# Kernel optimization log

Measured on AMD Instinct MI355X. Metric: run time of the kernel, lower is better.

## Reference

```python
import jax, jax.numpy as jnp
import numpy as np

M = 16                      # multiplicity of each irrep block
INV3 = 1.0 / np.sqrt(3.0)   # w3j(1,1,0) component-normalized
INV2 = 1.0 / np.sqrt(2.0)   # w3j(1,1,1) component-normalized
A0 = 1.0 / np.sqrt(2.0 * M) # fan-in norm for 0e outputs (2 paths x mul 16)
A1 = 1.0 / np.sqrt(3.0 * M) # fan-in norm for 1o outputs (3 paths x mul 16)


def setup_inputs() -> dict:
    E, N, ED, HID = 100000, 10000, 32, 128
    WNUM = 2 * M * (2 * M) + 3 * M * M  # 1792 per-edge TP weights
    ks = jax.random.split(jax.random.key(0), 10)
    return {
        "dst": jax.random.randint(ks[0], (E,), 0, N),
        "x_src": jax.random.normal(ks[1], (E, 4 * M), jnp.float32),   # 16x0e+16x1o
        "x_dst": jax.random.normal(ks[2], (N, 4 * M), jnp.float32),
        "sh": jax.random.normal(ks[3], (E, 4), jnp.float32),          # 1x0e+1x1o
        "edge_attr": jax.random.normal(ks[4], (E, ED), jnp.float32),
        "We1": jax.random.normal(ks[5], (ED, HID), jnp.float32) / np.sqrt(ED),
        "be1": jnp.zeros((HID,), jnp.float32),
        "We2": jax.random.normal(ks[6], (HID, WNUM), jnp.float32) / np.sqrt(HID),
        "be2": jnp.zeros((WNUM,), jnp.float32),
        "Wr0": jax.random.normal(ks[7], (M, 2 * M), jnp.float32),     # 16x0e -> 32x0e
        "Wr1": jax.random.normal(ks[8], (M, M), jnp.float32),         # 16x1o -> 16x1o
    }


def _forward(dst, x_src, x_dst, sh, edge_attr, We1, be1, We2, be2, Wr0, Wr1):
    E = x_src.shape[0]
    N = x_dst.shape[0]
    o0 = 2 * M  # 32x0e tp output (scalars + gates)

    # edge MLP -> per-edge tensor-product weights [E, 1792]
    w = jax.nn.relu(edge_attr @ We1 + be1) @ We2 + be2
    i = 0
    w_ss = w[:, i:i + M * o0].reshape(E, M, o0); i += M * o0   # 0e x 0e -> 0e
    w_vv0 = w[:, i:i + M * o0].reshape(E, M, o0); i += M * o0  # 1o x 1o -> 0e
    w_sv = w[:, i:i + M * M].reshape(E, M, M); i += M * M      # 0e x 1o -> 1o
    w_vs = w[:, i:i + M * M].reshape(E, M, M); i += M * M      # 1o x 0e -> 1o
    w_vv1 = w[:, i:i + M * M].reshape(E, M, M)                 # 1o x 1o -> 1o

    s1 = x_src[:, :M]                       # [E, 16]
    v1 = x_src[:, M:].reshape(E, M, 3)      # [E, 16, 3]
    s2 = sh[:, 0]                           # [E]
    v2 = sh[:, 1:4]                         # [E, 3]

    # fully-connected tensor product with per-edge weights
    out0 = A0 * (jnp.einsum('em,emo->eo', s1 * s2[:, None], w_ss)
                 + INV3 * jnp.einsum('emc,ec,emo->eo', v1, v2, w_vv0))  # [E, 32]
    cross = jnp.cross(v1, v2[:, None, :])   # [E, 16, 3]
    out1 = A1 * (jnp.einsum('em,ec,emo->eoc', s1, v2, w_sv)
                 + jnp.einsum('emc,e,emo->eoc', v1, s2, w_vs)
                 + INV2 * jnp.einsum('emc,emo->eoc', cross, w_vv1))     # [E, 16, 3]
    msg = jnp.concatenate([out0, out1.reshape(E, -1)], axis=1)          # [E, 80]

    # scatter-mean over destination nodes
    ssum = jax.ops.segment_sum(msg, dst, num_segments=N)
    cnt = jax.ops.segment_sum(jnp.ones((E,), msg.dtype), dst, num_segments=N)
    msg = ssum / jnp.maximum(cnt, 1.0)[:, None]                          # [N, 80]

    # residual equivariant linear on x_dst
    sd = x_dst[:, :M]
    vd = x_dst[:, M:].reshape(N, M, 3)
    res0 = (sd @ Wr0) / np.sqrt(M)                                       # [N, 32]
    res1 = jnp.einsum('nmc,mo->noc', vd, Wr1) / np.sqrt(M)               # [N, 16, 3]
    msg = msg + jnp.concatenate([res0, res1.reshape(N, -1)], axis=1)

    # gate nonlinearity: relu(scalars), sigmoid(gates) * gated vectors
    scalars = jax.nn.relu(msg[:, :M])
    gates = jax.nn.sigmoid(msg[:, M:2 * M])
    gated = msg[:, 2 * M:].reshape(N, M, 3) * gates[:, :, None]
    return jnp.concatenate([scalars, gated.reshape(N, -1)], axis=1)      # [N, 64]


def reference(dst, x_src, x_dst, sh, edge_attr, We1, be1, We2, be2, Wr0, Wr1):
    return _forward(dst, x_src, x_dst, sh, edge_attr, We1, be1, We2, be2, Wr0, Wr1)
```

## Files before the change

kernel.cpp:

```cpp
#include <hip/hip_runtime.h>
#include <math.h>

#define WNUM 1792
#define HID 128

#define INV3C 0.5773502691896258f
#define INV2C 0.7071067811865476f
#define A0C   0.17677669529663687f
#define A1C   0.14433756729740643f
#define MAXDEG 64

typedef short bf8 __attribute__((ext_vector_type(8)));
typedef _Float16 f16x8 __attribute__((ext_vector_type(8)));
typedef _Float16 f16x4 __attribute__((ext_vector_type(4)));
typedef float f32x4 __attribute__((ext_vector_type(4)));

__device__ inline unsigned short f2bf(float f) {
  union { float f; unsigned u; } v; v.f = f;
  unsigned r = v.u + 0x7FFFu + ((v.u >> 16) & 1u);
  return (unsigned short)(r >> 16);
}
__device__ inline float bf2f(unsigned short h) {
  union { unsigned u; float f; } v; v.u = ((unsigned)h) << 16;
  return v.f;
}
__device__ inline float wscale(int t) {
  if (t < 32) return A0C;
  if (t < 64) return A0C * INV3C;
  if (t < 96) return A1C;
  return A1C * INV2C;
}

__global__ __launch_bounds__(256) void prep_kernel(
    const float* __restrict__ We1, const float* __restrict__ We2,
    const float* __restrict__ be2,
    unsigned short* __restrict__ we1x, _Float16* __restrict__ we2h,
    float* __restrict__ be2p, int* __restrict__ cntp, int N)
{
  int i = blockIdx.x * 256 + threadIdx.x;
  if (i < 28672) {
    int t = i >> 8, c = (i >> 6) & 3, lane = i & 63;
    int quad = lane >> 4, l15 = lane & 15;
    int col = t * 16 + l15;
    float sc = wscale(t);
    f16x8 v;
    #pragma unroll
    for (int j = 0; j < 8; ++j) {
      int k = c * 32 + quad * 8 + j;
      v[j] = (_Float16)(We2[(size_t)k * WNUM + col] * sc);
    }
    *(f16x8*)(we2h + (size_t)t * 2048 + c * 512 + lane * 8) = v;
  } else if (i < 29184) {
    int q = i - 28672;
    int c1 = q >> 6, lane = q & 63;
    int quad = lane >> 4, l15 = lane & 15;
    int col = c1 * 16 + l15;
    bf8 hh, ll;
    #pragma unroll
    for (int j = 0; j < 8; ++j) {
      int k = quad * 8 + j;
      float v = We1[k * HID + col];
      unsigned short hi = f2bf(v);
      hh[j] = (short)hi;
      ll[j] = (short)f2bf(v - bf2f(hi));
    }
    *(bf8*)(we1x + c1 * 1024 + lane * 8) = hh;
    *(bf8*)(we1x + c1 * 1024 + 512 + lane * 8) = ll;
  } else if (i < 30976) {
    int q = i - 29184;
    int t = q >> 4, l16 = q & 15;
    be2p[(t >> 1) * 32 + l16 * 2 + (t & 1)] = be2[q] * wscale(t);
  } else if (i < 30976 + N) {
    cntp[i - 30976] = 0;
  }
}

__device__ inline void chains2(const f16x8* a0, const f16x8* a1,
    f16x8 b0, f16x8 b1, f16x8 b2, f16x8 b3,
    f16x8 b4, f16x8 b5, f16x8 b6, f16x8 b7,
    float2 bias, f32x4* wa, f32x4* wb)
{
  f32x4 ca0 = {bias.x, bias.x, bias.x, bias.x};
  f32x4 cb0 = {bias.y, bias.y, bias.y, bias.y};
  f32x4 ca1 = ca0, cb1 = cb0;
  ca0 = __builtin_amdgcn_mfma_f32_16x16x32_f16(a0[0], b0, ca0, 0, 0, 0);
  cb0 = __builtin_amdgcn_mfma_f32_16x16x32_f16(a0[0], b4, cb0, 0, 0, 0);
  ca1 = __builtin_amdgcn_mfma_f32_16x16x32_f16(a1[0], b0, ca1, 0, 0, 0);
  cb1 = __builtin_amdgcn_mfma_f32_16x16x32_f16(a1[0], b4, cb1, 0, 0, 0);
  ca0 = __builtin_amdgcn_mfma_f32_16x16x32_f16(a0[1], b1, ca0, 0, 0, 0);
  cb0 = __builtin_amdgcn_mfma_f32_16x16x32_f16(a0[1], b5, cb0, 0, 0, 0);
  ca1 = __builtin_amdgcn_mfma_f32_16x16x32_f16(a1[1], b1, ca1, 0, 0, 0);
  cb1 = __builtin_amdgcn_mfma_f32_16x16x32_f16(a1[1], b5, cb1, 0, 0, 0);
  ca0 = __builtin_amdgcn_mfma_f32_16x16x32_f16(a0[2], b2, ca0, 0, 0, 0);
  cb0 = __builtin_amdgcn_mfma_f32_16x16x32_f16(a0[2], b6, cb0, 0, 0, 0);
  ca1 = __builtin_amdgcn_mfma_f32_16x16x32_f16(a1[2], b2, ca1, 0, 0, 0);
  cb1 = __builtin_amdgcn_mfma_f32_16x16x32_f16(a1[2], b6, cb1, 0, 0, 0);
  ca0 = __builtin_amdgcn_mfma_f32_16x16x32_f16(a0[3], b3, ca0, 0, 0, 0);
  cb0 = __builtin_amdgcn_mfma_f32_16x16x32_f16(a0[3], b7, cb0, 0, 0, 0);
  ca1 = __builtin_amdgcn_mfma_f32_16x16x32_f16(a1[3], b3, ca1, 0, 0, 0);
  cb1 = __builtin_amdgcn_mfma_f32_16x16x32_f16(a1[3], b7, cb1, 0, 0, 0);
  wa[0] = ca0; wb[0] = cb0; wa[1] = ca1; wb[1] = cb1;
}

__device__ inline void pair_mm(const _Float16* bL, const float* bp, int p,
                               const f16x8 (&af)[2][4], f32x4* wa, f32x4* wb)
{
  f16x8 b0 = *(const f16x8*)(bL);
  f16x8 b1 = *(const f16x8*)(bL + 512);
  f16x8 b2 = *(const f16x8*)(bL + 1024);
  f16x8 b3 = *(const f16x8*)(bL + 1536);
  f16x8 b4 = *(const f16x8*)(bL + 2048);
  f16x8 b5 = *(const f16x8*)(bL + 2560);
  f16x8 b6 = *(const f16x8*)(bL + 3072);
  f16x8 b7 = *(const f16x8*)(bL + 3584);
  float2 bias2 = *(const float2*)(bp + p * 32);
  chains2(af[0], af[1], b0, b1, b2, b3, b4, b5, b6, b7, bias2, wa, wb);
}

template <bool MSG>
__global__ __launch_bounds__(512, 2) void edge_kernel(
    const float* __restrict__ ea, const float* __restrict__ xsrc,
    const float* __restrict__ sh, const int* __restrict__ dst,
    const float* __restrict__ be1,
    const unsigned short* __restrict__ we1x, const _Float16* __restrict__ we2h,
    const float* __restrict__ be2p,
    float* __restrict__ outp, int* __restrict__ eidx, int* __restrict__ cntp, int E)
{
  const int lane = threadIdx.x & 63;
  const int w    = threadIdx.x >> 6;
  const int quad = lane >> 4;
  const int l16  = lane & 15;
  const int eb   = (blockIdx.x * 8 + w) * 32;

  __shared__ union SMem {
    _Float16 h[8][16][136];
    _Float16 B[4][4096];
  } uS;
  __shared__ _Float16 s1h_s[8][16][32];
  __shared__ _Float16 v1h_s[8][16][3][32];
  __shared__ float4 vq_s[8][32];

  #define STAGE_PAIR(p) { \
    const _Float16* gsrc_ = we2h + (size_t)(p) * 4096; \
    _Float16* ldst_ = &uS.B[(p) & 3][0]; \
    __builtin_amdgcn_global_load_lds( \
      (const __attribute__((address_space(1))) void*)(gsrc_ + w * 512 + lane * 8), \
      (__attribute__((address_space(3))) void*)(ldst_ + w * 512), 16, 0, 0); \
  }

  if (lane < 32) {
    int ge = eb + lane;
    if (ge < E) {
      int node = dst[ge];
      int pos = atomicAdd(cntp + node, 1);
      if (MSG) { if (pos < MAXDEG) eidx[node * MAXDEG + pos] = ge; }
    }
  }

  {
    int e2 = lane >> 1, mg = lane & 1;
    int ge = eb + e2;
    if (ge < E) {
      const float* xp = xsrc + (size_t)ge * 64;
      float4 sq0 = *(const float4*)(xp + mg * 8);
      float4 sq1 = *(const float4*)(xp + mg * 8 + 4);
      float s1a[8] = {sq0.x,sq0.y,sq0.z,sq0.w,sq1.x,sq1.y,sq1.z,sq1.w};
      const float* vp = xp + 16 + mg * 24;
      float la[24];
      #pragma unroll
      for (int qv = 0; qv < 6; ++qv) {
        float4 t = *(const float4*)(vp + qv * 4);
        la[qv*4+0] = t.x; la[qv*4+1] = t.y; la[qv*4+2] = t.z; la[qv*4+3] = t.w;
      }
      float4 shq = *(const float4*)(sh + (size_t)ge * 4);
      float s2 = shq.x, v2x = shq.y, v2y = shq.z, v2z = shq.w;
      #pragma unroll
      for (int mi = 0; mi < 8; ++mi) {
        int m = mg * 8 + mi;
        float v1x = la[mi*3], v1y = la[mi*3+1], v1z = la[mi*3+2];
        s1h_s[w][m][e2] = (_Float16)s1a[mi];
        v1h_s[w][m][0][e2] = (_Float16)v1x;
        v1h_s[w][m][1][e2] = (_Float16)v1y;
        v1h_s[w][m][2][e2] = (_Float16)v1z;
      }
      if (mg == 0) vq_s[w][e2] = make_float4(v2x, v2y, v2z, s2);
    } else {
      #pragma unroll
      for (int mi = 0; mi < 8; ++mi) {
        int m = mg * 8 + mi;
        s1h_s[w][m][e2] = (_Float16)0.f;
        v1h_s[w][m][0][e2] = (_Float16)0.f;
        v1h_s[w][m][1][e2] = (_Float16)0.f;
        v1h_s[w][m][2][e2] = (_Float16)0.f;
      }
      if (mg == 0) vq_s[w][e2] = make_float4(0,0,0,0);
    }
  }

  f16x8 af[2][4];
  {
    const unsigned short* wb1 = we1x + lane * 8;
    #pragma unroll
    for (int g = 0; g < 2; ++g) {
      bf8 ah, al;
      {
        int gea = eb + g * 16 + l16; if (gea > E - 1) gea = E - 1;
        const float* ep = ea + (size_t)gea * 32 + quad * 8;
        float4 p0 = *(const float4*)ep;
        float4 p1 = *(const float4*)(ep + 4);
        float pv[8] = {p0.x,p0.y,p0.z,p0.w,p1.x,p1.y,p1.z,p1.w};
        #pragma unroll
        for (int j = 0; j < 8; ++j) {
          unsigned short hi = f2bf(pv[j]);
          ah[j] = (short)hi;
          al[j] = (short)f2bf(pv[j] - bf2f(hi));
        }
      }
      #pragma unroll 2
      for (int c = 0; c < 8; ++c) {
        bf8 bh = *(const bf8*)(wb1 + c * 1024);
        bf8 bl = *(const bf8*)(wb1 + c * 1024 + 512);
        float bias = be1[c * 16 + l16];
        f32x4 hc = {bias, bias, bias, bias};
        hc = __builtin_amdgcn_mfma_f32_16x16x32_bf16(al, bh, hc, 0, 0, 0);
        hc = __builtin_amdgcn_mfma_f32_16x16x32_bf16(ah, bl, hc, 0, 0, 0);
        hc = __builtin_amdgcn_mfma_f32_16x16x32_bf16(ah, bh, hc, 0, 0, 0);
        #pragma unroll
        for (int r = 0; r < 4; ++r)
          uS.h[w][quad * 4 + r][c * 16 + l16] = (_Float16)fmaxf(hc[r], 0.f);
      }
      #pragma unroll
      for (int ch = 0; ch < 4; ++ch)
        af[g][ch] = *(const f16x8*)&uS.h[w][l16][ch * 32 + quad * 8];
      asm volatile("s_waitcnt lgkmcnt(0)" ::: "memory");
      __builtin_amdgcn_sched_barrier(0);
    }
  }
  __syncthreads();

  STAGE_PAIR(0)
  STAGE_PAIR(1)
  __syncthreads();

  const float* bp = be2p + l16 * 2;
  float m0a[2][4] = {{0,0,0,0},{0,0,0,0}}, m0b[2][4] = {{0,0,0,0},{0,0,0,0}};

  {
    float s2v[2][4];
    #pragma unroll
    for (int g = 0; g < 2; ++g)
      #pragma unroll
      for (int r = 0; r < 4; ++r)
        s2v[g][r] = vq_s[w][g * 16 + quad * 4 + r].w;

    #pragma unroll 1
    for (int i = 0; i < 16; i += 2) {
      STAGE_PAIR(i + 2)
      STAGE_PAIR(i + 3)
      f32x4 wa[2], wb[2];
      pair_mm(&uS.B[i & 3][lane * 8], bp, i, af, wa, wb);
      #pragma unroll
      for (int g = 0; g < 2; ++g) {
        f16x4 fv = *(const f16x4*)&s1h_s[w][i][g * 16 + quad * 4];
        #pragma unroll
        for (int r = 0; r < 4; ++r) {
          float f = (float)fv[r] * s2v[g][r];
          m0a[g][r] = fmaf(wa[g][r], f, m0a[g][r]);
          m0b[g][r] = fmaf(wb[g][r], f, m0b[g][r]);
        }
      }
      pair_mm(&uS.B[(i + 1) & 3][lane * 8], bp, i + 1, af, wa, wb);
      #pragma unroll
      for (int g = 0; g < 2; ++g) {
        f16x4 fv = *(const f16x4*)&s1h_s[w][i + 1][g * 16 + quad * 4];
        #pragma unroll
        for (int r = 0; r < 4; ++r) {
          float f = (float)fv[r] * s2v[g][r];
          m0a[g][r] = fmaf(wa[g][r], f, m0a[g][r]);
          m0b[g][r] = fmaf(wb[g][r], f, m0b[g][r]);
        }
      }
      __syncthreads();
    }
  }

  {
    float v2xv[2][4], v2yv[2][4], v2zv[2][4];
    #pragma unroll
    for (int g = 0; g < 2; ++g)
      #pragma unroll
      for (int r = 0; r < 4; ++r) {
        float4 q = vq_s[w][g * 16 + quad * 4 + r];
        v2xv[g][r] = q.x; v2yv[g][r] = q.y; v2zv[g][r] = q.z;
      }

    #pragma unroll 1
    for (int i = 0; i < 16; i += 2) {
      int pg = 16 + i;
      STAGE_PAIR(pg + 2)
      STAGE_PAIR(pg + 3)
      f32x4 wa[2], wb[2];
      pair_mm(&uS.B[pg & 3][lane * 8], bp, pg, af, wa, wb);
      #pragma unroll
      for (int g = 0; g < 2; ++g) {
        f16x4 xA = *(const f16x4*)&v1h_s[w][i][0][g * 16 + quad * 4];
        f16x4 yA = *(const f16x4*)&v1h_s[w][i][1][g * 16 + quad * 4];
        f16x4 zA = *(const f16x4*)&v1h_s[w][i][2][g * 16 + quad * 4];
        #pragma unroll
        for (int r = 0; r < 4; ++r) {
          float f = fmaf((float)zA[r], v2zv[g][r],
                    fmaf((float)yA[r], v2yv[g][r], (float)xA[r] * v2xv[g][r]));
          m0a[g][r] = fmaf(wa[g][r], f, m0a[g][r]);
          m0b[g][r] = fmaf(wb[g][r], f, m0b[g][r]);
        }
      }
      pair_mm(&uS.B[(pg + 1) & 3][lane * 8], bp, pg + 1, af, wa, wb);
      #pragma unroll
      for (int g = 0; g < 2; ++g) {
        f16x4 xA = *(const f16x4*)&v1h_s[w][i + 1][0][g * 16 + quad * 4];
        f16x4 yA = *(const f16x4*)&v1h_s[w][i + 1][1][g * 16 + quad * 4];
        f16x4 zA = *(const f16x4*)&v1h_s[w][i + 1][2][g * 16 + quad * 4];
        #pragma unroll
        for (int r = 0; r < 4; ++r) {
          float f = fmaf((float)zA[r], v2zv[g][r],
                    fmaf((float)yA[r], v2yv[g][r], (float)xA[r] * v2xv[g][r]));
          m0a[g][r] = fmaf(wa[g][r], f, m0a[g][r]);
          m0b[g][r] = fmaf(wb[g][r], f, m0b[g][r]);
        }
      }
      __syncthreads();
    }
  }

  #pragma unroll
  for (int g = 0; g < 2; ++g)
    #pragma unroll
    for (int r = 0; r < 4; ++r) {
      int ge = eb + g * 16 + quad * 4 + r;
      if (ge < E) {
        if (MSG) {
          float* mp = outp + (size_t)ge * 80;
          mp[l16]      = m0a[g][r];
          mp[16 + l16] = m0b[g][r];
        } else {
          float* ap = outp + (size_t)dst[ge] * 80;
          atomicAdd(ap + l16,      m0a[g][r]);
          atomicAdd(ap + 16 + l16, m0b[g][r]);
        }
      }
    }

  float sg[2][4] = {{0,0,0,0},{0,0,0,0}};
  #pragma unroll 1
  for (int i = 0; i < 8; i += 2) {
    int pg = 32 + i;
    STAGE_PAIR(pg + 2)
    STAGE_PAIR(pg + 3)
    f32x4 wa[2], wb[2];
    pair_mm(&uS.B[pg & 3][lane * 8], bp, pg, af, wa, wb);
    #pragma unroll
    for (int g = 0; g < 2; ++g) {
      f16x4 sA = *(const f16x4*)&s1h_s[w][2*i][g * 16 + quad * 4];
      f16x4 sB = *(const f16x4*)&s1h_s[w][2*i + 1][g * 16 + quad * 4];
      #pragma unroll
      for (int r = 0; r < 4; ++r)
        sg[g][r] = fmaf(wb[g][r], (float)sB[r], fmaf(wa[g][r], (float)sA[r], sg[g][r]));
    }
    pair_mm(&uS.B[(pg + 1) & 3][lane * 8], bp, pg + 1, af, wa, wb);
    #pragma unroll
    for (int g = 0; g < 2; ++g) {
      f16x4 sA = *(const f16x4*)&s1h_s[w][2*i + 2][g * 16 + quad * 4];
      f16x4 sB = *(const f16x4*)&s1h_s[w][2*i + 3][g * 16 + quad * 4];
      #pragma unroll
      for (int r = 0; r < 4; ++r)
        sg[g][r] = fmaf(wb[g][r], (float)sB[r], fmaf(wa[g][r], (float)sA[r], sg[g][r]));
    }
    __syncthreads();
  }
  float4 vq[2][4];
  #pragma unroll
  for (int g = 0; g < 2; ++g)
    #pragma unroll
    for (int r = 0; r < 4; ++r) vq[g][r] = vq_s[w][g * 16 + quad * 4 + r];

  float m1x[2][4], m1y[2][4], m1z[2][4];
  #pragma unroll
  for (int g = 0; g < 2; ++g)
    #pragma unroll
    for (int r = 0; r < 4; ++r) {
      m1x[g][r] = sg[g][r] * vq[g][r].x;
      m1y[g][r] = sg[g][r] * vq[g][r].y;
      m1z[g][r] = sg[g][r] * vq[g][r].z;
    }

  #pragma unroll
  for (int sec = 0; sec < 2; ++sec) {
    float ux[2][4] = {{0,0,0,0},{0,0,0,0}}, uy[2][4] = {{0,0,0,0},{0,0,0,0}},
          uz[2][4] = {{0,0,0,0},{0,0,0,0}};
    int base = 40 + sec * 8;
    #pragma unroll 1
    for (int i = 0; i < 8; i += 2) {
      int pg = base + i;
      if (pg + 2 < 56) STAGE_PAIR(pg + 2)
      if (pg + 3 < 56) STAGE_PAIR(pg + 3)
      f32x4 wa[2], wb[2];
      pair_mm(&uS.B[pg & 3][lane * 8], bp, pg, af, wa, wb);
      #pragma unroll
      for (int g = 0; g < 2; ++g) {
        f16x4 xA = *(const f16x4*)&v1h_s[w][2*i][0][g*16 + quad*4];
        f16x4 xB = *(const f16x4*)&v1h_s[w][2*i+1][0][g*16 + quad*4];
        f16x4 yA = *(const f16x4*)&v1h_s[w][2*i][1][g*16 + quad*4];
        f16x4 yB = *(const f16x4*)&v1h_s[w][2*i+1][1][g*16 + quad*4];
        f16x4 zA = *(const f16x4*)&v1h_s[w][2*i][2][g*16 + quad*4];
        f16x4 zB = *(const f16x4*)&v1h_s[w][2*i+1][2][g*16 + quad*4];
        #pragma unroll
        for (int r = 0; r < 4; ++r) {
          ux[g][r] = fmaf(wb[g][r], (float)xB[r], fmaf(wa[g][r], (float)xA[r], ux[g][r]));
          uy[g][r] = fmaf(wb[g][r], (float)yB[r], fmaf(wa[g][r], (float)yA[r], uy[g][r]));
          uz[g][r] = fmaf(wb[g][r], (float)zB[r], fmaf(wa[g][r], (float)zA[r], uz[g][r]));
        }
      }
      pair_mm(&uS.B[(pg + 1) & 3][lane * 8], bp, pg + 1, af, wa, wb);
      #pragma unroll
      for (int g = 0; g < 2; ++g) {
        f16x4 xA = *(const f16x4*)&v1h_s[w][2*i+2][0][g*16 + quad*4];
        f16x4 xB = *(const f16x4*)&v1h_s[w][2*i+3][0][g*16 + quad*4];
        f16x4 yA = *(const f16x4*)&v1h_s[w][2*i+2][1][g*16 + quad*4];
        f16x4 yB = *(const f16x4*)&v1h_s[w][2*i+3][1][g*16 + quad*4];
        f16x4 zA = *(const f16x4*)&v1h_s[w][2*i+2][2][g*16 + quad*4];
        f16x4 zB = *(const f16x4*)&v1h_s[w][2*i+3][2][g*16 + quad*4];
        #pragma unroll
        for (int r = 0; r < 4; ++r) {
          ux[g][r] = fmaf(wb[g][r], (float)xB[r], fmaf(wa[g][r], (float)xA[r], ux[g][r]));
          uy[g][r] = fmaf(wb[g][r], (float)yB[r], fmaf(wa[g][r], (float)yA[r], uy[g][r]));
          uz[g][r] = fmaf(wb[g][r], (float)zB[r], fmaf(wa[g][r], (float)zA[r], uz[g][r]));
        }
      }
      __syncthreads();
    }
    if (sec == 0) {
      #pragma unroll
      for (int g = 0; g < 2; ++g)
        #pragma unroll
        for (int r = 0; r < 4; ++r) {
          m1x[g][r] = fmaf(vq[g][r].w, ux[g][r], m1x[g][r]);
          m1y[g][r] = fmaf(vq[g][r].w, uy[g][r], m1y[g][r]);
          m1z[g][r] = fmaf(vq[g][r].w, uz[g][r], m1z[g][r]);
        }
    } else {
      #pragma unroll
      for (int g = 0; g < 2; ++g)
        #pragma unroll
        for (int r = 0; r < 4; ++r) {
          m1x[g][r] = fmaf(uy[g][r], vq[g][r].z, m1x[g][r]);
          m1x[g][r] = fmaf(-uz[g][r], vq[g][r].y, m1x[g][r]);
          m1y[g][r] = fmaf(uz[g][r], vq[g][r].x, m1y[g][r]);
          m1y[g][r] = fmaf(-ux[g][r], vq[g][r].z, m1y[g][r]);
          m1z[g][r] = fmaf(ux[g][r], vq[g][r].y, m1z[g][r]);
          m1z[g][r] = fmaf(-uy[g][r], vq[g][r].x, m1z[g][r]);
        }
    }
  }

  #pragma unroll
  for (int g = 0; g < 2; ++g)
    #pragma unroll
    for (int r = 0; r < 4; ++r) {
      int ge = eb + g * 16 + quad * 4 + r;
      if (ge < E) {
        if (MSG) {
          float* mp = outp + (size_t)ge * 80;
          mp[32 + l16*3 + 0] = m1x[g][r];
          mp[32 + l16*3 + 1] = m1y[g][r];
          mp[32 + l16*3 + 2] = m1z[g][r];
        } else {
          float* ap = outp + (size_t)dst[ge] * 80;
          atomicAdd(ap + 32 + l16*3 + 0, m1x[g][r]);
          atomicAdd(ap + 32 + l16*3 + 1, m1y[g][r]);
          atomicAdd(ap + 32 + l16*3 + 2, m1z[g][r]);
        }
      }
    }
  #undef STAGE_PAIR
}

__global__ __launch_bounds__(128) void node_gather_kernel(
    const float* __restrict__ msg, const int* __restrict__ eidx,
    const int* __restrict__ cntp,
    const float* __restrict__ xdst, const float* __restrict__ Wr0,
    const float* __restrict__ Wr1, float* __restrict__ out, int N)
{
  int n = blockIdx.x;
  if (n >= N) return;
  int j = threadIdx.x;
  int c0 = cntp[n];
  int deg = c0 < MAXDEG ? c0 : MAXDEG;
  float inv = 1.0f / fmaxf((float)c0, 1.0f);
  __shared__ float s_sum[80];
  if (j < 80) {
    float s = 0.f;
    const int* ep = eidx + (size_t)n * MAXDEG;
    int i = 0;
    for (; i + 1 < deg; i += 2) {
      int e0 = ep[i], e1 = ep[i + 1];
      s += msg[(size_t)e0 * 80 + j] + msg[(size_t)e1 * 80 + j];
    }
    if (i < deg) s += msg[(size_t)ep[i] * 80 + j];
    s_sum[j] = s * inv;
  }
  __syncthreads();
  if (j >= 64) return;
  const float* xd = xdst + (size_t)n * 64;
  float* op = out + (size_t)n * 64;
  if (j < 16) {
    float s = 0.f;
    #pragma unroll
    for (int m = 0; m < 16; ++m) s = fmaf(xd[m], Wr0[m * 32 + j], s);
    op[j] = fmaxf(s_sum[j] + 0.25f * s, 0.f);
  } else {
    int jj = j - 16;
    int o = (jj * 86) >> 8;
    int c = jj - o * 3;
    float tg = 0.f, v = 0.f;
    #pragma unroll
    for (int m = 0; m < 16; ++m) {
      tg = fmaf(xd[m], Wr0[m * 32 + 16 + o], tg);
      v  = fmaf(xd[16 + m * 3 + c], Wr1[m * 16 + o], v);
    }
    float g = 1.0f / (1.0f + expf(-(s_sum[16 + o] + 0.25f * tg)));
    op[16 + jj] = (s_sum[32 + jj] + 0.25f * v) * g;
  }
}

__global__ __launch_bounds__(256) void node_kernel(
    const float* __restrict__ accn, const int* __restrict__ cntp,
    const float* __restrict__ xdst, const float* __restrict__ Wr0,
    const float* __restrict__ Wr1, float* __restrict__ out, int N)
{
  int idx = blockIdx.x * 256 + threadIdx.x;
  int n = idx >> 6, j = idx & 63;
  if (n >= N) return;
  float inv = 1.0f / fmaxf((float)cntp[n], 1.0f);
  const float* ap = accn + (size_t)n * 80;
  const float* xd = xdst + (size_t)n * 64;
  float* op = out + (size_t)n * 64;
  if (j < 16) {
    float s = 0.f;
    #pragma unroll
    for (int m = 0; m < 16; ++m) s = fmaf(xd[m], Wr0[m * 32 + j], s);
    op[j] = fmaxf(ap[j] * inv + 0.25f * s, 0.f);
  } else {
    int jj = j - 16;
    int o = (jj * 86) >> 8;
    int c = jj - o * 3;
    float tg = 0.f, v = 0.f;
    #pragma unroll
    for (int m = 0; m < 16; ++m) {
      tg = fmaf(xd[m], Wr0[m * 32 + 16 + o], tg);
      v  = fmaf(xd[16 + m * 3 + c], Wr1[m * 16 + o], v);
    }
    float g = 1.0f / (1.0f + expf(-(ap[16 + o] * inv + 0.25f * tg)));
    op[16 + jj] = (ap[32 + jj] * inv + 0.25f * v) * g;
  }
}

extern "C" void kernel_launch(void* const* d_in, const int* in_sizes, int n_in,
                              void* d_out, int out_size, void* d_ws, size_t ws_size,
                              hipStream_t stream)
{
  const int*   dst  = (const int*)d_in[0];
  const float* xsrc = (const float*)d_in[1];
  const float* xdst = (const float*)d_in[2];
  const float* sh   = (const float*)d_in[3];
  const float* ea   = (const float*)d_in[4];
  const float* We1  = (const float*)d_in[5];
  const float* be1  = (const float*)d_in[6];
  const float* We2  = (const float*)d_in[7];
  const float* be2  = (const float*)d_in[8];
  const float* Wr0  = (const float*)d_in[9];
  const float* Wr1  = (const float*)d_in[10];
  const int E = in_sizes[0];
  const int N = in_sizes[2] / 64;

  char* ws = (char*)d_ws;
  _Float16* we2h = (_Float16*)ws;
  unsigned short* we1x = (unsigned short*)(ws + 458752);
  float* be2p = (float*)(ws + 475136);
  int*   cntp = (int*)(ws + 482560);
  size_t off = 482560 + (size_t)N * 4;
  off = (off + 15) & ~(size_t)15;

  size_t need_msg = off + (size_t)N * MAXDEG * 4 + (size_t)E * 80 * 4;
  bool use_msg = (ws_size >= need_msg);

  prep_kernel<<<(30976 + N + 255) / 256, 256, 0, stream>>>(We1, We2, be2,
      we1x, we2h, be2p, cntp, N);

  if (use_msg) {
    int* eidx = (int*)(ws + off);
    float* msg = (float*)(ws + off + (size_t)N * MAXDEG * 4);
    edge_kernel<true><<<(E + 255) / 256, 512, 0, stream>>>(ea, xsrc, sh, dst, be1,
        we1x, we2h, be2p, msg, eidx, cntp, E);
    node_gather_kernel<<<N, 128, 0, stream>>>(msg, eidx, cntp, xdst, Wr0, Wr1,
        (float*)d_out, N);
  } else {
    float* accn = (float*)(ws + off);
    hipMemsetAsync(accn, 0, (size_t)N * 320, stream);
    edge_kernel<false><<<(E + 255) / 256, 512, 0, stream>>>(ea, xsrc, sh, dst, be1,
        we1x, we2h, be2p, accn, (int*)nullptr, cntp, E);
    node_kernel<<<((size_t)N * 64 + 255) / 256, 256, 0, stream>>>(accn, cntp,
        xdst, Wr0, Wr1, (float*)d_out, N);
  }
}
```

Baseline: 206.4 us.

## Read We2 tiles directly from global memory instead of LDS staging, halve block size

Drops the cooperative global_load_lds staging of the per-edge TP weight matrix (We2) into a four-slot LDS ring buffer. Each wave now loads its B fragments straight from global memory, relying on L1/L2 caching of the small shared weight table. This removes the per-iteration __syncthreads barriers and frees the staging LDS. Blocks shrink from 8 to 4 waves to raise occupancy and scheduling flexibility. The cost is more global and cache traffic per wave and exposed load latency before each MFMA chain, since there is no longer any software prefetch.

```diff
diff --git a/kernel.cpp b/kernel.cpp
--- a/kernel.cpp
+++ b/kernel.cpp
@@ -102,23 +102,23 @@
   wa[0] = ca0; wb[0] = cb0; wa[1] = ca1; wb[1] = cb1;
 }
 
-__device__ inline void pair_mm(const _Float16* bL, const float* bp, int p,
+__device__ inline void pair_mm(const _Float16* __restrict__ bG, const float* bp, int p,
                                const f16x8 (&af)[2][4], f32x4* wa, f32x4* wb)
 {
-  f16x8 b0 = *(const f16x8*)(bL);
-  f16x8 b1 = *(const f16x8*)(bL + 512);
-  f16x8 b2 = *(const f16x8*)(bL + 1024);
-  f16x8 b3 = *(const f16x8*)(bL + 1536);
-  f16x8 b4 = *(const f16x8*)(bL + 2048);
-  f16x8 b5 = *(const f16x8*)(bL + 2560);
-  f16x8 b6 = *(const f16x8*)(bL + 3072);
-  f16x8 b7 = *(const f16x8*)(bL + 3584);
+  f16x8 b0 = *(const f16x8*)(bG);
+  f16x8 b1 = *(const f16x8*)(bG + 512);
+  f16x8 b2 = *(const f16x8*)(bG + 1024);
+  f16x8 b3 = *(const f16x8*)(bG + 1536);
+  f16x8 b4 = *(const f16x8*)(bG + 2048);
+  f16x8 b5 = *(const f16x8*)(bG + 2560);
+  f16x8 b6 = *(const f16x8*)(bG + 3072);
+  f16x8 b7 = *(const f16x8*)(bG + 3584);
   float2 bias2 = *(const float2*)(bp + p * 32);
   chains2(af[0], af[1], b0, b1, b2, b3, b4, b5, b6, b7, bias2, wa, wb);
 }
 
 template <bool MSG>
-__global__ __launch_bounds__(512, 2) void edge_kernel(
+__global__ __launch_bounds__(256, 2) void edge_kernel(
     const float* __restrict__ ea, const float* __restrict__ xsrc,
     const float* __restrict__ sh, const int* __restrict__ dst,
     const float* __restrict__ be1,
@@ -130,23 +130,12 @@
   const int w    = threadIdx.x >> 6;
   const int quad = lane >> 4;
   const int l16  = lane & 15;
-  const int eb   = (blockIdx.x * 8 + w) * 32;
-
-  __shared__ union SMem {
-    _Float16 h[8][16][136];
-    _Float16 B[4][4096];
-  } uS;
-  __shared__ _Float16 s1h_s[8][16][32];
-  __shared__ _Float16 v1h_s[8][16][3][32];
-  __shared__ float4 vq_s[8][32];
-
-  #define STAGE_PAIR(p) { \
-    const _Float16* gsrc_ = we2h + (size_t)(p) * 4096; \
-    _Float16* ldst_ = &uS.B[(p) & 3][0]; \
-    __builtin_amdgcn_global_load_lds( \
-      (const __attribute__((address_space(1))) void*)(gsrc_ + w * 512 + lane * 8), \
-      (__attribute__((address_space(3))) void*)(ldst_ + w * 512), 16, 0, 0); \
-  }
+  const int eb   = (blockIdx.x * 4 + w) * 32;
+
+  __shared__ _Float16 h_s[4][16][136];
+  __shared__ _Float16 s1h_s[4][16][32];
+  __shared__ _Float16 v1h_s[4][16][3][32];
+  __shared__ float4 vq_s[4][32];
 
   if (lane < 32) {
     int ge = eb + lane;
@@ -227,22 +216,18 @@
         hc = __builtin_amdgcn_mfma_f32_16x16x32_bf16(ah, bh, hc, 0, 0, 0);
         #pragma unroll
         for (int r = 0; r < 4; ++r)
-          uS.h[w][quad * 4 + r][c * 16 + l16] = (_Float16)fmaxf(hc[r], 0.f);
+          h_s[w][quad * 4 + r][c * 16 + l16] = (_Float16)fmaxf(hc[r], 0.f);
       }
       #pragma unroll
       for (int ch = 0; ch < 4; ++ch)
-        af[g][ch] = *(const f16x8*)&uS.h[w][l16][ch * 32 + quad * 8];
+        af[g][ch] = *(const f16x8*)&h_s[w][l16][ch * 32 + quad * 8];
       asm volatile("s_waitcnt lgkmcnt(0)" ::: "memory");
       __builtin_amdgcn_sched_barrier(0);
     }
   }
-  __syncthreads();
-
-  STAGE_PAIR(0)
-  STAGE_PAIR(1)
-  __syncthreads();
 
   const float* bp = be2p + l16 * 2;
+  const _Float16* bG0 = we2h + lane * 8;
   float m0a[2][4] = {{0,0,0,0},{0,0,0,0}}, m0b[2][4] = {{0,0,0,0},{0,0,0,0}};
 
   {
@@ -255,10 +240,8 @@
 
     #pragma unroll 1
     for (int i = 0; i < 16; i += 2) {
-      STAGE_PAIR(i + 2)
-      STAGE_PAIR(i + 3)
       f32x4 wa[2], wb[2];
-      pair_mm(&uS.B[i & 3][lane * 8], bp, i, af, wa, wb);
+      pair_mm(bG0 + (size_t)i * 4096, bp, i, af, wa, wb);
       #pragma unroll
       for (int g = 0; g < 2; ++g) {
         f16x4 fv = *(const f16x4*)&s1h_s[w][i][g * 16 + quad * 4];
@@ -269,7 +252,7 @@
           m0b[g][r] = fmaf(wb[g][r], f, m0b[g][r]);
         }
       }
-      pair_mm(&uS.B[(i + 1) & 3][lane * 8], bp, i + 1, af, wa, wb);
+      pair_mm(bG0 + (size_t)(i + 1) * 4096, bp, i + 1, af, wa, wb);
       #pragma unroll
       for (int g = 0; g < 2; ++g) {
         f16x4 fv = *(const f16x4*)&s1h_s[w][i + 1][g * 16 + quad * 4];
@@ -280,7 +263,6 @@
           m0b[g][r] = fmaf(wb[g][r], f, m0b[g][r]);
         }
       }
-      __syncthreads();
     }
   }
 
@@ -297,10 +279,8 @@
     #pragma unroll 1
     for (int i = 0; i < 16; i += 2) {
       int pg = 16 + i;
-      STAGE_PAIR(pg + 2)
-      STAGE_PAIR(pg + 3)
       f32x4 wa[2], wb[2];
-      pair_mm(&uS.B[pg & 3][lane * 8], bp, pg, af, wa, wb);
+      pair_mm(bG0 + (size_t)pg * 4096, bp, pg, af, wa, wb);
       #pragma unroll
       for (int g = 0; g < 2; ++g) {
         f16x4 xA = *(const f16x4*)&v1h_s[w][i][0][g * 16 + quad * 4];
@@ -314,7 +294,7 @@
           m0b[g][r] = fmaf(wb[g][r], f, m0b[g][r]);
         }
       }
-      pair_mm(&uS.B[(pg + 1) & 3][lane * 8], bp, pg + 1, af, wa, wb);
+      pair_mm(bG0 + (size_t)(pg + 1) * 4096, bp, pg + 1, af, wa, wb);
       #pragma unroll
       for (int g = 0; g < 2; ++g) {
         f16x4 xA = *(const f16x4*)&v1h_s[w][i + 1][0][g * 16 + quad * 4];
@@ -328,7 +308,6 @@
           m0b[g][r] = fmaf(wb[g][r], f, m0b[g][r]);
         }
       }
-      __syncthreads();
     }
   }
 
@@ -354,10 +333,8 @@
   #pragma unroll 1
   for (int i = 0; i < 8; i += 2) {
     int pg = 32 + i;
-    STAGE_PAIR(pg + 2)
-    STAGE_PAIR(pg + 3)
     f32x4 wa[2], wb[2];
-    pair_mm(&uS.B[pg & 3][lane * 8], bp, pg, af, wa, wb);
+    pair_mm(bG0 + (size_t)pg * 4096, bp, pg, af, wa, wb);
     #pragma unroll
     for (int g = 0; g < 2; ++g) {
       f16x4 sA = *(const f16x4*)&s1h_s[w][2*i][g * 16 + quad * 4];
@@ -366,7 +343,7 @@
       for (int r = 0; r < 4; ++r)
         sg[g][r] = fmaf(wb[g][r], (float)sB[r], fmaf(wa[g][r], (float)sA[r], sg[g][r]));
     }
-    pair_mm(&uS.B[(pg + 1) & 3][lane * 8], bp, pg + 1, af, wa, wb);
+    pair_mm(bG0 + (size_t)(pg + 1) * 4096, bp, pg + 1, af, wa, wb);
     #pragma unroll
     for (int g = 0; g < 2; ++g) {
       f16x4 sA = *(const f16x4*)&s1h_s[w][2*i + 2][g * 16 + quad * 4];
@@ -375,7 +352,6 @@
       for (int r = 0; r < 4; ++r)
         sg[g][r] = fmaf(wb[g][r], (float)sB[r], fmaf(wa[g][r], (float)sA[r], sg[g][r]));
     }
-    __syncthreads();
   }
   float4 vq[2][4];
   #pragma unroll
@@ -401,10 +377,8 @@
     #pragma unroll 1
     for (int i = 0; i < 8; i += 2) {
       int pg = base + i;
-      if (pg + 2 < 56) STAGE_PAIR(pg + 2)
-      if (pg + 3 < 56) STAGE_PAIR(pg + 3)
       f32x4 wa[2], wb[2];
-      pair_mm(&uS.B[pg & 3][lane * 8], bp, pg, af, wa, wb);
+      pair_mm(bG0 + (size_t)pg * 4096, bp, pg, af, wa, wb);
       #pragma unroll
       for (int g = 0; g < 2; ++g) {
         f16x4 xA = *(const f16x4*)&v1h_s[w][2*i][0][g*16 + quad*4];
@@ -420,7 +394,7 @@
           uz[g][r] = fmaf(wb[g][r], (float)zB[r], fmaf(wa[g][r], (float)zA[r], uz[g][r]));
         }
       }
-      pair_mm(&uS.B[(pg + 1) & 3][lane * 8], bp, pg + 1, af, wa, wb);
+      pair_mm(bG0 + (size_t)(pg + 1) * 4096, bp, pg + 1, af, wa, wb);
       #pragma unroll
       for (int g = 0; g < 2; ++g) {
         f16x4 xA = *(const f16x4*)&v1h_s[w][2*i+2][0][g*16 + quad*4];
@@ -436,7 +410,6 @@
           uz[g][r] = fmaf(wb[g][r], (float)zB[r], fmaf(wa[g][r], (float)zA[r], uz[g][r]));
         }
       }
-      __syncthreads();
     }
     if (sec == 0) {
       #pragma unroll
@@ -481,7 +454,6 @@
         }
       }
     }
-  #undef STAGE_PAIR
 }
 
 __global__ __launch_bounds__(128) void node_gather_kernel(
@@ -599,14 +571,14 @@
   if (use_msg) {
     int* eidx = (int*)(ws + off);
     float* msg = (float*)(ws + off + (size_t)N * MAXDEG * 4);
-    edge_kernel<true><<<(E + 255) / 256, 512, 0, stream>>>(ea, xsrc, sh, dst, be1,
+    edge_kernel<true><<<(E + 127) / 128, 256, 0, stream>>>(ea, xsrc, sh, dst, be1,
         we1x, we2h, be2p, msg, eidx, cntp, E);
     node_gather_kernel<<<N, 128, 0, stream>>>(msg, eidx, cntp, xdst, Wr0, Wr1,
         (float*)d_out, N);
   } else {
     float* accn = (float*)(ws + off);
     hipMemsetAsync(accn, 0, (size_t)N * 320, stream);
-    edge_kernel<false><<<(E + 255) / 256, 512, 0, stream>>>(ea, xsrc, sh, dst, be1,
+    edge_kernel<false><<<(E + 127) / 128, 256, 0, stream>>>(ea, xsrc, sh, dst, be1,
         we1x, we2h, be2p, accn, (int*)nullptr, cntp, E);
     node_kernel<<<((size_t)N * 64 + 255) / 256, 256, 0, stream>>>(accn, cntp,
         xdst, Wr0, Wr1, (float*)d_out, N);
```

After: 201.0 us. -2.6%, faster.
